# Kernel optimization log

Hardware: AMD Instinct MI355X
Metric: run time of the kernel (lower is better)

## Reference

```python
import jax, jax.numpy as jnp
import numpy as np

N = 1024
D = 64

def setup_inputs() -> dict:
    key = jax.random.key(0)
    ks = jax.random.split(key, 8)
    s = lambda k, shp, fan: jax.random.normal(k, shp, dtype=jnp.float32) * (1.0 / np.sqrt(fan))
    return {
        "cell_states": jax.random.normal(ks[0], (N, D), dtype=jnp.float32),
        "adjacency": jax.random.uniform(ks[1], (N, N), dtype=jnp.float32) * 0.1,
        "gate_w1": s(ks[2], (64, 2 * D), 2 * D),
        "gate_b1": jnp.zeros((64,), jnp.float32),
        "gate_w2": s(ks[3], (32, 64), 64),
        "gate_b2": jnp.zeros((32,), jnp.float32),
        "gate_w3": s(ks[4], (1, 32), 32),
        "gate_b3": jnp.zeros((1,), jnp.float32),
        "sig_w": s(ks[5], (D, D), D),
        "sig_b": jnp.zeros((D,), jnp.float32),
    }

def reference(cell_states, adjacency, gate_w1, gate_b1, gate_w2, gate_b2,
              gate_w3, gate_b3, sig_w, sig_b):
    n = cell_states.shape[0]
    eye = jnp.eye(n, dtype=cell_states.dtype)
    # symmetrize, zero diagonal, row-softmax (diagonal zeros still participate in softmax)
    sym_adj = 0.5 * (adjacency + adjacency.T) * (1.0 - eye)
    norm_adj = jax.nn.softmax(sym_adj, axis=1)  # [N, N]
    # gate MLP on concat(x_i, x_j): split first linear to avoid materializing [N,N,2D]
    w1a, w1b = gate_w1[:, :D], gate_w1[:, D:]
    hi = cell_states @ w1a.T          # [N, 64] contribution of own state i
    hj = cell_states @ w1b.T          # [N, 64] contribution of other state j
    h1 = jax.nn.relu(hi[:, None, :] + hj[None, :, :] + gate_b1)   # [N, N, 64]
    h2 = jax.nn.relu(jnp.einsum('ijk,hk->ijh', h1, gate_w2) + gate_b2)  # [N, N, 32]
    gate = jax.nn.sigmoid(jnp.einsum('ijh,oh->ijo', h2, gate_w3) + gate_b3)[..., 0]  # [N, N]
    transferred = cell_states @ sig_w.T + sig_b   # [N, D]
    # exclude i == j pairs (loop skips them)
    weight = gate * norm_adj * (1.0 - eye)        # [N, N]
    return cell_states + weight @ transferred     # [N, D]
```

## Files before the change

kernel.cpp:

```cpp
#include <hip/hip_runtime.h>
#include <hip/hip_bf16.h>

#define N 1024
#define D 64

typedef __attribute__((ext_vector_type(8))) short bf16x8;
typedef __attribute__((ext_vector_type(16))) float f32x16;

__device__ __forceinline__ short f2bf(float x) {
    __hip_bfloat16 b = __float2bfloat16(x);
    return __builtin_bit_cast(short, b);
}

__global__ __launch_bounds__(256) void precompute_kernel(
    const float* __restrict__ cell, const float* __restrict__ w1,
    const float* __restrict__ b1, const float* __restrict__ sw,
    const float* __restrict__ sb,
    float* __restrict__ hi, float* __restrict__ hjb, float* __restrict__ trf)
{
    __shared__ float w1s[64 * 129];
    __shared__ float sws[64 * 65];
    __shared__ float xs[4 * 64];
    const int t = threadIdx.x;
    const int b = blockIdx.x;
    #pragma unroll
    for (int k = 0; k < 8; k++) {
        int f4 = t + 256 * k;
        int row = f4 >> 5, c4 = (f4 & 31) * 4;
        float4 v = *(const float4*)&w1[(size_t)row * 128 + c4];
        w1s[row * 129 + c4 + 0] = v.x;
        w1s[row * 129 + c4 + 1] = v.y;
        w1s[row * 129 + c4 + 2] = v.z;
        w1s[row * 129 + c4 + 3] = v.w;
    }
    #pragma unroll
    for (int k = 0; k < 4; k++) {
        int f4 = t + 256 * k;
        int row = f4 >> 4, c4 = (f4 & 15) * 4;
        float4 v = *(const float4*)&sw[(size_t)row * 64 + c4];
        sws[row * 65 + c4 + 0] = v.x;
        sws[row * 65 + c4 + 1] = v.y;
        sws[row * 65 + c4 + 2] = v.z;
        sws[row * 65 + c4 + 3] = v.w;
    }
    xs[t] = cell[(size_t)b * 256 + t];
    __syncthreads();
    const int wv = t >> 6, l = t & 63;
    const float* xr = &xs[wv * 64];
    float a0 = 0.0f, a1 = 0.0f, a2 = 0.0f;
    #pragma unroll 16
    for (int d = 0; d < 64; d++) {
        float x = xr[d];
        a0 = fmaf(x, w1s[l * 129 + d], a0);
        a1 = fmaf(x, w1s[l * 129 + 64 + d], a1);
        a2 = fmaf(x, sws[l * 65 + d], a2);
    }
    const int i = b * 4 + wv;
    hi[(size_t)i * D + l]  = a0;
    hjb[(size_t)i * D + l] = a1 + b1[l];
    trf[(size_t)i * D + l] = a2 + sb[l];
}

__global__ __launch_bounds__(256, 3) void gate_fused_kernel(
    const float* __restrict__ A, const float* __restrict__ hi,
    const float* __restrict__ hjb, const float* __restrict__ trf,
    const float* __restrict__ w2, const float* __restrict__ b2,
    const float* __restrict__ w3, const float* __restrict__ b3,
    float* __restrict__ part, float* __restrict__ rsp)
{
    __shared__ float smem[8352];
    float* S1    = smem;
    float* T2    = smem + 2048;
    float* hjb_s = smem + 4128;
    const int t   = threadIdx.x;
    const int w   = t >> 6;
    const int l   = t & 63;
    const int i0  = blockIdx.x * 32;
    const int by  = blockIdx.y;
    const int jb0 = by * 64;
    const int jbase = jb0 + w * 16;
    const int p   = l & 31;
    const int hi8 = l >> 5;
    const int i_mine = i0 + p;

    #pragma unroll
    for (int k = 0; k < 4; k++) {
        int f4 = t + 256 * k;
        *(float4*)&hjb_s[f4 * 4] = *(const float4*)&hjb[(size_t)jb0 * D + f4 * 4];
    }
    #pragma unroll
    for (int k = 0; k < 2; k++) {
        int f4 = t + 256 * k;
        int row = f4 >> 3, c4 = (f4 & 7) * 4;
        *(float4*)&S1[row * 32 + c4] =
            *(const float4*)&A[(size_t)(jb0 + row) * N + i0 + c4];
    }
    #pragma unroll
    for (int k = 0; k < 2; k++) {
        int f4 = t + 256 * k;
        int r = f4 >> 4, c4 = (f4 & 15) * 4;
        float4 v = *(const float4*)&A[(size_t)(i0 + r) * N + jb0 + c4];
        T2[r * 65 + c4 + 0] = v.x;
        T2[r * 65 + c4 + 1] = v.y;
        T2[r * 65 + c4 + 2] = v.z;
        T2[r * 65 + c4 + 3] = v.w;
    }

    float hv[32];
    #pragma unroll
    for (int q = 0; q < 4; q++) {
        float4 v0 = *(const float4*)&hi[(size_t)i_mine * D + q * 16 + hi8 * 8];
        float4 v1 = *(const float4*)&hi[(size_t)i_mine * D + q * 16 + hi8 * 8 + 4];
        hv[q * 8 + 0] = v0.x; hv[q * 8 + 1] = v0.y;
        hv[q * 8 + 2] = v0.z; hv[q * 8 + 3] = v0.w;
        hv[q * 8 + 4] = v1.x; hv[q * 8 + 5] = v1.y;
        hv[q * 8 + 6] = v1.z; hv[q * 8 + 7] = v1.w;
    }
    bf16x8 wa[4];
    #pragma unroll
    for (int q = 0; q < 4; q++) {
        const float* wp = &w2[(size_t)p * D + q * 16 + hi8 * 8];
        #pragma unroll
        for (int e = 0; e < 8; e++) wa[q][e] = f2bf(wp[e]);
    }
    float b2r[16], w3r[16];
    #pragma unroll
    for (int r = 0; r < 16; r++) {
        int ch = (r & 3) + 8 * (r >> 2) + 4 * hi8;
        b2r[r] = b2[ch];
        w3r[r] = w3[ch];
    }
    const float b3v = b3[0];

    __syncthreads();

    bf16x8 wf = {0, 0, 0, 0, 0, 0, 0, 0};
    float es = 0.0f;
    #pragma unroll
    for (int jj = 0; jj < 16; jj++) {
        const int jl = w * 16 + jj;
        const int j  = jb0 + jl;
        bf16x8 bq[4];
        #pragma unroll
        for (int q = 0; q < 4; q++) {
            float4 h0 = *(const float4*)&hjb_s[jl * 64 + q * 16 + hi8 * 8];
            float4 h1 = *(const float4*)&hjb_s[jl * 64 + q * 16 + hi8 * 8 + 4];
            bq[q][0] = f2bf(fmaxf(hv[q * 8 + 0] + h0.x, 0.0f));
            bq[q][1] = f2bf(fmaxf(hv[q * 8 + 1] + h0.y, 0.0f));
            bq[q][2] = f2bf(fmaxf(hv[q * 8 + 2] + h0.z, 0.0f));
            bq[q][3] = f2bf(fmaxf(hv[q * 8 + 3] + h0.w, 0.0f));
            bq[q][4] = f2bf(fmaxf(hv[q * 8 + 4] + h1.x, 0.0f));
            bq[q][5] = f2bf(fmaxf(hv[q * 8 + 5] + h1.y, 0.0f));
            bq[q][6] = f2bf(fmaxf(hv[q * 8 + 6] + h1.z, 0.0f));
            bq[q][7] = f2bf(fmaxf(hv[q * 8 + 7] + h1.w, 0.0f));
        }
        f32x16 accA, accB;
        #pragma unroll
        for (int r = 0; r < 16; r++) { accA[r] = b2r[r]; accB[r] = 0.0f; }
        accA = __builtin_amdgcn_mfma_f32_32x32x16_bf16(wa[0], bq[0], accA, 0, 0, 0);
        accA = __builtin_amdgcn_mfma_f32_32x32x16_bf16(wa[1], bq[1], accA, 0, 0, 0);
        accB = __builtin_amdgcn_mfma_f32_32x32x16_bf16(wa[2], bq[2], accB, 0, 0, 0);
        accB = __builtin_amdgcn_mfma_f32_32x32x16_bf16(wa[3], bq[3], accB, 0, 0, 0);

        float gp = 0.0f;
        #pragma unroll
        for (int r = 0; r < 16; r++)
            gp = fmaf(fmaxf(accA[r] + accB[r], 0.0f), w3r[r], gp);
        gp += __shfl_xor(gp, 32);

        const bool isdiag = (i_mine == j);
        float sym  = 0.5f * (S1[jl * 32 + p] + T2[p * 65 + jl]);
        float e    = isdiag ? 1.0f : __expf(sym);
        float gate = 1.0f / (1.0f + __expf(-(gp + b3v)));
        float u    = isdiag ? 0.0f : gate * e;
        if ((jj >> 3) == hi8) es += e;
        short ub = f2bf(u);
        wf[jj & 7] = ((jj >> 3) == hi8) ? ub : wf[jj & 7];
    }
    es += __shfl_xor(es, 32);

    bf16x8 tf0, tf1;
    #pragma unroll
    for (int e8 = 0; e8 < 8; e8++) {
        const float* tp = &trf[(size_t)(jbase + hi8 * 8 + e8) * D];
        tf0[e8] = f2bf(tp[p]);
        tf1[e8] = f2bf(tp[32 + p]);
    }
    f32x16 oA, oB;
    #pragma unroll
    for (int r = 0; r < 16; r++) { oA[r] = 0.0f; oB[r] = 0.0f; }
    oA = __builtin_amdgcn_mfma_f32_32x32x16_bf16(wf, tf0, oA, 0, 0, 0);
    oB = __builtin_amdgcn_mfma_f32_32x32x16_bf16(wf, tf1, oB, 0, 0, 0);

    __syncthreads();
    float* red = smem;
    float* esb = smem + 8192;
    #pragma unroll
    for (int r = 0; r < 16; r++) {
        int row = (r & 3) + 8 * (r >> 2) + 4 * hi8;
        red[w * 2048 + row * 64 + p]      = oA[r];
        red[w * 2048 + row * 64 + 32 + p] = oB[r];
    }
    if (hi8 == 0) esb[w * 32 + p] = es;
    __syncthreads();
    #pragma unroll
    for (int e = 0; e < 8; e++) {
        int idx = t + e * 256;
        float s = red[idx] + red[2048 + idx] + red[4096 + idx] + red[6144 + idx];
        part[(size_t)by * (N * D) + (size_t)i0 * D + idx] = s;
    }
    if (t < 32)
        rsp[by * N + i0 + t] = esb[t] + esb[32 + t] + esb[64 + t] + esb[96 + t];
}

__global__ __launch_bounds__(256) void finish_kernel(
    const float* __restrict__ cell, const float* __restrict__ part,
    const float* __restrict__ rsp, float* __restrict__ out)
{
    const int idx = blockIdx.x * 256 + threadIdx.x;
    const int i = idx >> 6;
    float rs = 0.0f;
    #pragma unroll
    for (int k = 0; k < 16; k++) rs += rsp[k * N + i];
    float acc = 0.0f;
    #pragma unroll
    for (int k = 0; k < 16; k++) acc += part[(size_t)k * (N * D) + idx];
    out[idx] = cell[idx] + acc / rs;
}

extern "C" void kernel_launch(void* const* d_in, const int* in_sizes, int n_in,
                              void* d_out, int out_size, void* d_ws, size_t ws_size,
                              hipStream_t stream) {
    const float* cell = (const float*)d_in[0];
    const float* adj  = (const float*)d_in[1];
    const float* w1   = (const float*)d_in[2];
    const float* b1   = (const float*)d_in[3];
    const float* w2   = (const float*)d_in[4];
    const float* b2   = (const float*)d_in[5];
    const float* w3   = (const float*)d_in[6];
    const float* b3   = (const float*)d_in[7];
    const float* sw   = (const float*)d_in[8];
    const float* sb   = (const float*)d_in[9];
    float* out = (float*)d_out;

    float* ws    = (float*)d_ws;
    float* hi    = ws;
    float* hjb   = hi + N * D;
    float* trf   = hjb + N * D;
    float* part  = trf + N * D;
    float* rsp   = part + (size_t)N * D * 16;

    precompute_kernel<<<256, 256, 0, stream>>>(cell, w1, b1, sw, sb, hi, hjb, trf);
    gate_fused_kernel<<<dim3(32, 16), 256, 0, stream>>>(adj, hi, hjb, trf,
                                                        w2, b2, w3, b3,
                                                        part, rsp);
    finish_kernel<<<256, 256, 0, stream>>>(cell, part, rsp, out);
}
```

Measured before the change: 31.70 us.

## Store hi/hj/trf as packed bf16 and halve j-tile per gate block

The precompute kernel now writes hi, hj and the transferred features as packed bf16, so the gate kernel reads half the bytes and builds MFMA fragments with packed adds. The j-tile per block shrinks from 64 to 32 and the grid doubles to 32x32, with launch bounds raised to 4 waves/SIMD for more parallelism. The adjacency transpose tile is stored transposed in LDS, and the second and third layers use paired float ops. In exchange, the finish kernel must reduce twice as many partial slices, which doubles partial-buffer traffic. hi and hj are now rounded to bf16 before the add, which adds precision loss.

```diff
diff --git a/kernel.cpp b/kernel.cpp
--- a/kernel.cpp
+++ b/kernel.cpp
@@ -6,17 +6,31 @@
 
 typedef __attribute__((ext_vector_type(8))) short bf16x8;
 typedef __attribute__((ext_vector_type(16))) float f32x16;
-
-__device__ __forceinline__ short f2bf(float x) {
+typedef __attribute__((ext_vector_type(2))) float f32x2;
+
+__device__ __forceinline__ unsigned short f2bf(float x) {
     __hip_bfloat16 b = __float2bfloat16(x);
-    return __builtin_bit_cast(short, b);
+    return (unsigned short)__builtin_bit_cast(short, b);
+}
+
+__device__ __forceinline__ unsigned h1p(unsigned a, unsigned b) {
+    f32x2 av, bv;
+    av.x = __builtin_bit_cast(float, a << 16);
+    av.y = __builtin_bit_cast(float, a & 0xffff0000u);
+    bv.x = __builtin_bit_cast(float, b << 16);
+    bv.y = __builtin_bit_cast(float, b & 0xffff0000u);
+    f32x2 s = av + bv;
+    f32x2 z = {0.0f, 0.0f};
+    s = __builtin_elementwise_max(s, z);
+    return (unsigned)f2bf(s.x) | ((unsigned)f2bf(s.y) << 16);
 }
 
 __global__ __launch_bounds__(256) void precompute_kernel(
     const float* __restrict__ cell, const float* __restrict__ w1,
     const float* __restrict__ b1, const float* __restrict__ sw,
     const float* __restrict__ sb,
-    float* __restrict__ hi, float* __restrict__ hjb, float* __restrict__ trf)
+    unsigned* __restrict__ hih, unsigned* __restrict__ hjbh,
+    unsigned short* __restrict__ trfb)
 {
     __shared__ float w1s[64 * 129];
     __shared__ float sws[64 * 65];
@@ -56,135 +70,143 @@
         a2 = fmaf(x, sws[l * 65 + d], a2);
     }
     const int i = b * 4 + wv;
-    hi[(size_t)i * D + l]  = a0;
-    hjb[(size_t)i * D + l] = a1 + b1[l];
-    trf[(size_t)i * D + l] = a2 + sb[l];
-}
-
-__global__ __launch_bounds__(256, 3) void gate_fused_kernel(
-    const float* __restrict__ A, const float* __restrict__ hi,
-    const float* __restrict__ hjb, const float* __restrict__ trf,
+    unsigned s0 = f2bf(a0);
+    unsigned s1 = f2bf(a1 + b1[l]);
+    unsigned p0 = (unsigned)__shfl_xor((int)s0, 1);
+    unsigned p1 = (unsigned)__shfl_xor((int)s1, 1);
+    if (!(l & 1)) {
+        hih [i * 32 + (l >> 1)] = s0 | (p0 << 16);
+        hjbh[i * 32 + (l >> 1)] = s1 | (p1 << 16);
+    }
+    trfb[i * 64 + l] = f2bf(a2 + sb[l]);
+}
+
+__global__ __launch_bounds__(256, 4) void gate_fused_kernel(
+    const float* __restrict__ A, const unsigned* __restrict__ hih,
+    const unsigned* __restrict__ hjbh, const unsigned short* __restrict__ trfb,
     const float* __restrict__ w2, const float* __restrict__ b2,
     const float* __restrict__ w3, const float* __restrict__ b3,
     float* __restrict__ part, float* __restrict__ rsp)
 {
-    __shared__ float smem[8352];
-    float* S1    = smem;
-    float* T2    = smem + 2048;
-    float* hjb_s = smem + 4128;
+    __shared__ float smem[8320];
+    unsigned* hjbh_s = (unsigned*)smem;
+    float*    S1     = smem + 1024;
+    float*    T2t    = smem + 2048;
     const int t   = threadIdx.x;
     const int w   = t >> 6;
     const int l   = t & 63;
     const int i0  = blockIdx.x * 32;
     const int by  = blockIdx.y;
-    const int jb0 = by * 64;
-    const int jbase = jb0 + w * 16;
+    const int jb0 = by * 32;
     const int p   = l & 31;
     const int hi8 = l >> 5;
     const int i_mine = i0 + p;
 
-    #pragma unroll
-    for (int k = 0; k < 4; k++) {
-        int f4 = t + 256 * k;
-        *(float4*)&hjb_s[f4 * 4] = *(const float4*)&hjb[(size_t)jb0 * D + f4 * 4];
-    }
-    #pragma unroll
-    for (int k = 0; k < 2; k++) {
-        int f4 = t + 256 * k;
-        int row = f4 >> 3, c4 = (f4 & 7) * 4;
+    {
+        int row = t >> 3, c4 = (t & 7) * 4;
+        *(uint4*)&hjbh_s[row * 32 + c4] =
+            *(const uint4*)&hjbh[(size_t)(jb0 + row) * 32 + c4];
         *(float4*)&S1[row * 32 + c4] =
             *(const float4*)&A[(size_t)(jb0 + row) * N + i0 + c4];
-    }
-    #pragma unroll
-    for (int k = 0; k < 2; k++) {
-        int f4 = t + 256 * k;
-        int r = f4 >> 4, c4 = (f4 & 15) * 4;
-        float4 v = *(const float4*)&A[(size_t)(i0 + r) * N + jb0 + c4];
-        T2[r * 65 + c4 + 0] = v.x;
-        T2[r * 65 + c4 + 1] = v.y;
-        T2[r * 65 + c4 + 2] = v.z;
-        T2[r * 65 + c4 + 3] = v.w;
-    }
-
-    float hv[32];
+        float4 v = *(const float4*)&A[(size_t)(i0 + row) * N + jb0 + c4];
+        T2t[(c4 + 0) * 33 + row] = v.x;
+        T2t[(c4 + 1) * 33 + row] = v.y;
+        T2t[(c4 + 2) * 33 + row] = v.z;
+        T2t[(c4 + 3) * 33 + row] = v.w;
+    }
+
+    uint4 hvb[4];
+    #pragma unroll
+    for (int q = 0; q < 4; q++)
+        hvb[q] = *(const uint4*)&hih[(size_t)i_mine * 32 + q * 8 + hi8 * 4];
+
+    bf16x8 wa[4];
     #pragma unroll
     for (int q = 0; q < 4; q++) {
-        float4 v0 = *(const float4*)&hi[(size_t)i_mine * D + q * 16 + hi8 * 8];
-        float4 v1 = *(const float4*)&hi[(size_t)i_mine * D + q * 16 + hi8 * 8 + 4];
-        hv[q * 8 + 0] = v0.x; hv[q * 8 + 1] = v0.y;
-        hv[q * 8 + 2] = v0.z; hv[q * 8 + 3] = v0.w;
-        hv[q * 8 + 4] = v1.x; hv[q * 8 + 5] = v1.y;
-        hv[q * 8 + 6] = v1.z; hv[q * 8 + 7] = v1.w;
-    }
-    bf16x8 wa[4];
-    #pragma unroll
-    for (int q = 0; q < 4; q++) {
-        const float* wp = &w2[(size_t)p * D + q * 16 + hi8 * 8];
-        #pragma unroll
-        for (int e = 0; e < 8; e++) wa[q][e] = f2bf(wp[e]);
-    }
-    float b2r[16], w3r[16];
-    #pragma unroll
-    for (int r = 0; r < 16; r++) {
-        int ch = (r & 3) + 8 * (r >> 2) + 4 * hi8;
-        b2r[r] = b2[ch];
-        w3r[r] = w3[ch];
+        float4 v0 = *(const float4*)&w2[(size_t)p * D + q * 16 + hi8 * 8];
+        float4 v1 = *(const float4*)&w2[(size_t)p * D + q * 16 + hi8 * 8 + 4];
+        wa[q][0] = (short)f2bf(v0.x); wa[q][1] = (short)f2bf(v0.y);
+        wa[q][2] = (short)f2bf(v0.z); wa[q][3] = (short)f2bf(v0.w);
+        wa[q][4] = (short)f2bf(v1.x); wa[q][5] = (short)f2bf(v1.y);
+        wa[q][6] = (short)f2bf(v1.z); wa[q][7] = (short)f2bf(v1.w);
+    }
+    f32x2 b2v[8], w3v[8];
+    #pragma unroll
+    for (int g = 0; g < 4; g++) {
+        float4 qb = *(const float4*)&b2[g * 8 + hi8 * 4];
+        float4 qw = *(const float4*)&w3[g * 8 + hi8 * 4];
+        b2v[2 * g].x = qb.x;     b2v[2 * g].y = qb.y;
+        b2v[2 * g + 1].x = qb.z; b2v[2 * g + 1].y = qb.w;
+        w3v[2 * g].x = qw.x;     w3v[2 * g].y = qw.y;
+        w3v[2 * g + 1].x = qw.z; w3v[2 * g + 1].y = qw.w;
     }
     const float b3v = b3[0];
+    const bool wsel = ((w & 1) == hi8);
 
     __syncthreads();
 
     bf16x8 wf = {0, 0, 0, 0, 0, 0, 0, 0};
     float es = 0.0f;
     #pragma unroll
-    for (int jj = 0; jj < 16; jj++) {
-        const int jl = w * 16 + jj;
+    for (int jj = 0; jj < 8; jj++) {
+        const int jl = w * 8 + jj;
         const int j  = jb0 + jl;
-        bf16x8 bq[4];
+
+        f32x16 accA, accB;
+        #pragma unroll
+        for (int r2 = 0; r2 < 8; r2++) {
+            accA[2 * r2] = b2v[r2].x; accA[2 * r2 + 1] = b2v[r2].y;
+            accB[2 * r2] = 0.0f;      accB[2 * r2 + 1] = 0.0f;
+        }
         #pragma unroll
         for (int q = 0; q < 4; q++) {
-            float4 h0 = *(const float4*)&hjb_s[jl * 64 + q * 16 + hi8 * 8];
-            float4 h1 = *(const float4*)&hjb_s[jl * 64 + q * 16 + hi8 * 8 + 4];
-            bq[q][0] = f2bf(fmaxf(hv[q * 8 + 0] + h0.x, 0.0f));
-            bq[q][1] = f2bf(fmaxf(hv[q * 8 + 1] + h0.y, 0.0f));
-            bq[q][2] = f2bf(fmaxf(hv[q * 8 + 2] + h0.z, 0.0f));
-            bq[q][3] = f2bf(fmaxf(hv[q * 8 + 3] + h0.w, 0.0f));
-            bq[q][4] = f2bf(fmaxf(hv[q * 8 + 4] + h1.x, 0.0f));
-            bq[q][5] = f2bf(fmaxf(hv[q * 8 + 5] + h1.y, 0.0f));
-            bq[q][6] = f2bf(fmaxf(hv[q * 8 + 6] + h1.z, 0.0f));
-            bq[q][7] = f2bf(fmaxf(hv[q * 8 + 7] + h1.w, 0.0f));
+            uint4 hb4 = *(const uint4*)&hjbh_s[jl * 32 + q * 8 + hi8 * 4];
+            uint4 fr;
+            fr.x = h1p(hvb[q].x, hb4.x);
+            fr.y = h1p(hvb[q].y, hb4.y);
+            fr.z = h1p(hvb[q].z, hb4.z);
+            fr.w = h1p(hvb[q].w, hb4.w);
+            bf16x8 frag = __builtin_bit_cast(bf16x8, fr);
+            if (q < 2)
+                accA = __builtin_amdgcn_mfma_f32_32x32x16_bf16(wa[q], frag, accA, 0, 0, 0);
+            else
+                accB = __builtin_amdgcn_mfma_f32_32x32x16_bf16(wa[q], frag, accB, 0, 0, 0);
         }
-        f32x16 accA, accB;
+
+        f32x2 g0 = {0.0f, 0.0f}, g1 = {0.0f, 0.0f};
+        f32x2 z2 = {0.0f, 0.0f};
         #pragma unroll
-        for (int r = 0; r < 16; r++) { accA[r] = b2r[r]; accB[r] = 0.0f; }
-        accA = __builtin_amdgcn_mfma_f32_32x32x16_bf16(wa[0], bq[0], accA, 0, 0, 0);
-        accA = __builtin_amdgcn_mfma_f32_32x32x16_bf16(wa[1], bq[1], accA, 0, 0, 0);
-        accB = __builtin_amdgcn_mfma_f32_32x32x16_bf16(wa[2], bq[2], accB, 0, 0, 0);
-        accB = __builtin_amdgcn_mfma_f32_32x32x16_bf16(wa[3], bq[3], accB, 0, 0, 0);
-
-        float gp = 0.0f;
-        #pragma unroll
-        for (int r = 0; r < 16; r++)
-            gp = fmaf(fmaxf(accA[r] + accB[r], 0.0f), w3r[r], gp);
+        for (int r2 = 0; r2 < 8; r2++) {
+            f32x2 s;
+            s.x = accA[2 * r2] + accB[2 * r2];
+            s.y = accA[2 * r2 + 1] + accB[2 * r2 + 1];
+            s = __builtin_elementwise_max(s, z2);
+            if (r2 & 1) g1 = __builtin_elementwise_fma(s, w3v[r2], g1);
+            else        g0 = __builtin_elementwise_fma(s, w3v[r2], g0);
+        }
+        g0 += g1;
+        float gp = g0.x + g0.y;
         gp += __shfl_xor(gp, 32);
 
         const bool isdiag = (i_mine == j);
-        float sym  = 0.5f * (S1[jl * 32 + p] + T2[p * 65 + jl]);
+        float sym  = 0.5f * (S1[jl * 32 + p] + T2t[jl * 33 + p]);
         float e    = isdiag ? 1.0f : __expf(sym);
         float gate = 1.0f / (1.0f + __expf(-(gp + b3v)));
         float u    = isdiag ? 0.0f : gate * e;
-        if ((jj >> 3) == hi8) es += e;
-        short ub = f2bf(u);
-        wf[jj & 7] = ((jj >> 3) == hi8) ? ub : wf[jj & 7];
+        if ((jj >> 2) == hi8) es += e;
+        short ub = (short)f2bf(u);
+        wf[jj] = wsel ? ub : wf[jj];
     }
     es += __shfl_xor(es, 32);
 
+    const int grp = w >> 1;
     bf16x8 tf0, tf1;
     #pragma unroll
     for (int e8 = 0; e8 < 8; e8++) {
-        const float* tp = &trf[(size_t)(jbase + hi8 * 8 + e8) * D];
-        tf0[e8] = f2bf(tp[p]);
-        tf1[e8] = f2bf(tp[32 + p]);
+        const unsigned short* tp =
+            &trfb[(size_t)(jb0 + grp * 16 + hi8 * 8 + e8) * 64];
+        tf0[e8] = (short)tp[p];
+        tf1[e8] = (short)tp[32 + p];
     }
     f32x16 oA, oB;
     #pragma unroll
@@ -221,10 +243,10 @@
     const int i = idx >> 6;
     float rs = 0.0f;
     #pragma unroll
-    for (int k = 0; k < 16; k++) rs += rsp[k * N + i];
+    for (int k = 0; k < 32; k++) rs += rsp[k * N + i];
     float acc = 0.0f;
     #pragma unroll
-    for (int k = 0; k < 16; k++) acc += part[(size_t)k * (N * D) + idx];
+    for (int k = 0; k < 32; k++) acc += part[(size_t)k * (N * D) + idx];
     out[idx] = cell[idx] + acc / rs;
 }
 
@@ -243,15 +265,15 @@
     const float* sb   = (const float*)d_in[9];
     float* out = (float*)d_out;
 
-    float* ws    = (float*)d_ws;
-    float* hi    = ws;
-    float* hjb   = hi + N * D;
-    float* trf   = hjb + N * D;
-    float* part  = trf + N * D;
-    float* rsp   = part + (size_t)N * D * 16;
-
-    precompute_kernel<<<256, 256, 0, stream>>>(cell, w1, b1, sw, sb, hi, hjb, trf);
-    gate_fused_kernel<<<dim3(32, 16), 256, 0, stream>>>(adj, hi, hjb, trf,
+    unsigned*       hih  = (unsigned*)d_ws;
+    unsigned*       hjbh = hih + N * 32;
+    unsigned short* trfb = (unsigned short*)(hjbh + N * 32);
+    float*          part = (float*)(trfb + N * 64);
+    float*          rsp  = part + (size_t)32 * N * D;
+
+    precompute_kernel<<<256, 256, 0, stream>>>(cell, w1, b1, sw, sb,
+                                               hih, hjbh, trfb);
+    gate_fused_kernel<<<dim3(32, 32), 256, 0, stream>>>(adj, hih, hjbh, trfb,
                                                         w2, b2, w3, b3,
                                                         part, rsp);
     finish_kernel<<<256, 256, 0, stream>>>(cell, part, rsp, out);
```

After: 38.65 us. 1.22x slower.

## Double gate kernel block to 512 threads, halving j-columns per wave

Applied to the files above, without the earlier changes.

The gate kernel now runs 8 waves per block instead of 4, with each wave handling 8 j columns instead of 16. Pairs of waves share one 16-column MFMA tile for the final weight×transferred product, selected by wave parity. The cross-wave reduction grows to 8 partials and shared memory roughly doubles. This raises per-CU parallelism and shortens the serial per-wave loop, at the cost of more redundant per-wave setup (hi, w2 loads) and a bigger reduction. The gate dot product is also split into two accumulators to shorten the FMA dependency chain.

```diff
diff --git a/kernel.cpp b/kernel.cpp
--- a/kernel.cpp
+++ b/kernel.cpp
@@ -61,44 +61,39 @@
     trf[(size_t)i * D + l] = a2 + sb[l];
 }
 
-__global__ __launch_bounds__(256, 3) void gate_fused_kernel(
+__global__ __launch_bounds__(512, 4) void gate_fused_kernel(
     const float* __restrict__ A, const float* __restrict__ hi,
     const float* __restrict__ hjb, const float* __restrict__ trf,
     const float* __restrict__ w2, const float* __restrict__ b2,
     const float* __restrict__ w3, const float* __restrict__ b3,
     float* __restrict__ part, float* __restrict__ rsp)
 {
-    __shared__ float smem[8352];
-    float* S1    = smem;
-    float* T2    = smem + 2048;
-    float* hjb_s = smem + 4128;
+    __shared__ float smem[16640];
+    float* hjb_s = smem;
+    float* S1    = smem + 4096;
+    float* T2    = smem + 6144;
     const int t   = threadIdx.x;
     const int w   = t >> 6;
     const int l   = t & 63;
     const int i0  = blockIdx.x * 32;
     const int by  = blockIdx.y;
     const int jb0 = by * 64;
-    const int jbase = jb0 + w * 16;
     const int p   = l & 31;
     const int hi8 = l >> 5;
     const int i_mine = i0 + p;
 
     #pragma unroll
-    for (int k = 0; k < 4; k++) {
-        int f4 = t + 256 * k;
+    for (int k = 0; k < 2; k++) {
+        int f4 = t + 512 * k;
         *(float4*)&hjb_s[f4 * 4] = *(const float4*)&hjb[(size_t)jb0 * D + f4 * 4];
     }
-    #pragma unroll
-    for (int k = 0; k < 2; k++) {
-        int f4 = t + 256 * k;
-        int row = f4 >> 3, c4 = (f4 & 7) * 4;
+    {
+        int row = t >> 3, c4 = (t & 7) * 4;
         *(float4*)&S1[row * 32 + c4] =
             *(const float4*)&A[(size_t)(jb0 + row) * N + i0 + c4];
     }
-    #pragma unroll
-    for (int k = 0; k < 2; k++) {
-        int f4 = t + 256 * k;
-        int r = f4 >> 4, c4 = (f4 & 15) * 4;
+    {
+        int r = t >> 4, c4 = (t & 15) * 4;
         float4 v = *(const float4*)&A[(size_t)(i0 + r) * N + jb0 + c4];
         T2[r * 65 + c4 + 0] = v.x;
         T2[r * 65 + c4 + 1] = v.y;
@@ -130,15 +125,16 @@
         b2r[r] = b2[ch];
         w3r[r] = w3[ch];
     }
-    const float b3v = b3[0];
+    const float b3v  = b3[0];
+    const bool  wsel = (hi8 == (w & 1));
 
     __syncthreads();
 
     bf16x8 wf = {0, 0, 0, 0, 0, 0, 0, 0};
     float es = 0.0f;
     #pragma unroll
-    for (int jj = 0; jj < 16; jj++) {
-        const int jl = w * 16 + jj;
+    for (int jj = 0; jj < 8; jj++) {
+        const int jl = w * 8 + jj;
         const int j  = jb0 + jl;
         bf16x8 bq[4];
         #pragma unroll
@@ -162,10 +158,13 @@
         accB = __builtin_amdgcn_mfma_f32_32x32x16_bf16(wa[2], bq[2], accB, 0, 0, 0);
         accB = __builtin_amdgcn_mfma_f32_32x32x16_bf16(wa[3], bq[3], accB, 0, 0, 0);
 
-        float gp = 0.0f;
-        #pragma unroll
-        for (int r = 0; r < 16; r++)
-            gp = fmaf(fmaxf(accA[r] + accB[r], 0.0f), w3r[r], gp);
+        float gp0 = 0.0f, gp1 = 0.0f;
+        #pragma unroll
+        for (int r = 0; r < 16; r += 2) {
+            gp0 = fmaf(fmaxf(accA[r] + accB[r], 0.0f), w3r[r], gp0);
+            gp1 = fmaf(fmaxf(accA[r + 1] + accB[r + 1], 0.0f), w3r[r + 1], gp1);
+        }
+        float gp = gp0 + gp1;
         gp += __shfl_xor(gp, 32);
 
         const bool isdiag = (i_mine == j);
@@ -173,16 +172,17 @@
         float e    = isdiag ? 1.0f : __expf(sym);
         float gate = 1.0f / (1.0f + __expf(-(gp + b3v)));
         float u    = isdiag ? 0.0f : gate * e;
-        if ((jj >> 3) == hi8) es += e;
+        if (wsel) es += e;
         short ub = f2bf(u);
-        wf[jj & 7] = ((jj >> 3) == hi8) ? ub : wf[jj & 7];
+        wf[jj] = wsel ? ub : wf[jj];
     }
     es += __shfl_xor(es, 32);
 
+    const int grp = w >> 1;
     bf16x8 tf0, tf1;
     #pragma unroll
     for (int e8 = 0; e8 < 8; e8++) {
-        const float* tp = &trf[(size_t)(jbase + hi8 * 8 + e8) * D];
+        const float* tp = &trf[(size_t)(jb0 + grp * 16 + hi8 * 8 + e8) * D];
         tf0[e8] = f2bf(tp[p]);
         tf1[e8] = f2bf(tp[32 + p]);
     }
@@ -194,7 +194,7 @@
 
     __syncthreads();
     float* red = smem;
-    float* esb = smem + 8192;
+    float* esb = smem + 16384;
     #pragma unroll
     for (int r = 0; r < 16; r++) {
         int row = (r & 3) + 8 * (r >> 2) + 4 * hi8;
@@ -204,13 +204,19 @@
     if (hi8 == 0) esb[w * 32 + p] = es;
     __syncthreads();
     #pragma unroll
-    for (int e = 0; e < 8; e++) {
-        int idx = t + e * 256;
-        float s = red[idx] + red[2048 + idx] + red[4096 + idx] + red[6144 + idx];
+    for (int e = 0; e < 4; e++) {
+        int idx = t + e * 512;
+        float s = 0.0f;
+        #pragma unroll
+        for (int ww = 0; ww < 8; ww++) s += red[ww * 2048 + idx];
         part[(size_t)by * (N * D) + (size_t)i0 * D + idx] = s;
     }
-    if (t < 32)
-        rsp[by * N + i0 + t] = esb[t] + esb[32 + t] + esb[64 + t] + esb[96 + t];
+    if (t < 32) {
+        float s = 0.0f;
+        #pragma unroll
+        for (int ww = 0; ww < 8; ww++) s += esb[ww * 32 + t];
+        rsp[by * N + i0 + t] = s;
+    }
 }
 
 __global__ __launch_bounds__(256) void finish_kernel(
@@ -251,7 +257,7 @@
     float* rsp   = part + (size_t)N * D * 16;
 
     precompute_kernel<<<256, 256, 0, stream>>>(cell, w1, b1, sw, sb, hi, hjb, trf);
-    gate_fused_kernel<<<dim3(32, 16), 256, 0, stream>>>(adj, hi, hjb, trf,
+    gate_fused_kernel<<<dim3(32, 16), 512, 0, stream>>>(adj, hi, hjb, trf,
                                                         w2, b2, w3, b3,
                                                         part, rsp);
     finish_kernel<<<256, 256, 0, stream>>>(cell, part, rsp, out);
```

New measurement: 39.33 us. 24.1% more time.
